# Performance work log

Hardware: AMD Instinct MI355X
Metric: run time of the kernel (lower is better)

Reference implementation:

```python
import jax, jax.numpy as jnp
import numpy as np

STRIDE = 4
NUM_HEADS = 8


def _make_window(x, stride, nh):
    # (B,C,H,W) -> (B, nh, S, S, (H/S)*(W/S), C/nh)
    b, c, h, w = x.shape
    x = x.reshape(b, nh, c // nh, h // stride, stride, w // stride, stride)
    x = x.transpose(0, 1, 4, 6, 3, 5, 2)
    return x.reshape(b, nh, stride, stride, (h // stride) * (w // stride), c // nh)


def _demake_window(x, h, w):
    # (B, nh, S, S, L, dh) -> (B, nh*dh, H, W)
    b, nh, s, _, L, dh = x.shape
    x = x.reshape(b, nh, s, s, h // s, w // s, dh)
    x = x.transpose(0, 1, 6, 4, 2, 5, 3)
    return x.reshape(b, nh * dh, h, w)


def _proj(x, W, bias):
    # 1x1 conv == per-pixel GEMM: (B,C,H,W),(O,C) -> (B,O,H,W)
    return jnp.einsum('bchw,oc->bohw', x, W) + bias[None, :, None, None]


def setup_inputs() -> dict:
    key = jax.random.key(0)
    ks = jax.random.split(key, 12)
    B, C, H, W = 4, 256, 64, 64
    P, V, O = 256, 256, 256  # proj/value/out channels
    inp = {
        'fea_q': jax.random.normal(ks[0], (B, C, H, W), jnp.float32),
        'fea_k': jax.random.normal(ks[1], (B, C, H, W), jnp.float32),
        'fea_v': jax.random.normal(ks[2], (B, V, H, W), jnp.float32),
        'mask_q': (jax.random.uniform(ks[3], (B, 1, H, W)) > 0.5).astype(jnp.float32),
        'mask_k': (jax.random.uniform(ks[4], (B, 1, H, W)) > 0.5).astype(jnp.float32),
        'q_w': jax.random.normal(ks[5], (P, C), jnp.float32) * 0.02,
        'q_b': jnp.zeros((P,), jnp.float32),
        'k_w': jax.random.normal(ks[6], (P, C), jnp.float32) * 0.02,
        'k_b': jnp.zeros((P,), jnp.float32),
        'v_w': jax.random.normal(ks[7], (O, V), jnp.float32) * 0.02,
        'v_b': jnp.zeros((O,), jnp.float32),
    }
    return inp


def reference(fea_q, fea_k, fea_v, mask_q, mask_k, q_w, q_b, k_w, k_b, v_w, v_b):
    B, _, H, W = fea_q.shape
    head_dim = q_w.shape[0] // NUM_HEADS
    scaling = head_dim ** (-0.5)

    query = _make_window(_proj(fea_q, q_w, q_b), STRIDE, NUM_HEADS)
    key = _make_window(_proj(fea_k, k_w, k_b), STRIDE, NUM_HEADS)
    value = _make_window(_proj(fea_v, v_w, v_b), STRIDE, NUM_HEADS)

    # (B, nh, S, S, L, L)
    weights = jnp.matmul(query, jnp.swapaxes(key, -1, -2)) * scaling

    # mask attention (no-grad in original)
    mq = _make_window(jax.lax.stop_gradient(mask_q), STRIDE, 1)
    mk = _make_window(jax.lax.stop_gradient(mask_k), STRIDE, 1)
    mask_attn = jnp.matmul(mq, jnp.swapaxes(mk, -1, -2))  # (B,1,S,S,L,L)
    mask_sum = jnp.sum(mask_attn, axis=-1, keepdims=True)
    mask_attn = mask_attn + (mask_sum == 0).astype(jnp.float32)
    mask_attn = jnp.where(mask_attn == 0, -jnp.inf,
                          jnp.where(mask_attn == 1, 0.0, mask_attn))
    weights = weights + mask_attn

    weights = jax.nn.softmax(weights, axis=-1)  # dropout p=0 -> identity
    weights = weights * (1.0 - (mask_sum == 0).astype(jnp.float32))

    out = jnp.matmul(weights, value)  # (B, nh, S, S, L, dh)
    return _demake_window(out, H, W)
```

## Files before the change

### kernel.cpp

```cpp
#include <hip/hip_runtime.h>
#include <hip/hip_bf16.h>

#define NH 8
#define DH 32
#define LW 256
#define HW 4096
#define CIN 256

typedef float f32x4 __attribute__((ext_vector_type(4)));
typedef short s16x8 __attribute__((ext_vector_type(8)));
typedef short s16x4 __attribute__((ext_vector_type(4)));

#define AS1 __attribute__((address_space(1)))
#define AS3 __attribute__((address_space(3)))

__device__ __forceinline__ short f2bf(float f) {
  __hip_bfloat16 h = __float2bfloat16(f);
  short s; __builtin_memcpy(&s, &h, 2); return s;
}

__device__ __forceinline__ void gload_lds16(const void* g, void* l) {
  __builtin_amdgcn_global_load_lds((const AS1 void*)g, (AS3 void*)l, 16, 0, 0);
}

#define KOFF 4194304
#define VOFF 8388608
#define WTOFF 12582912

__global__ void wconv_kernel(const float* __restrict__ qw, const float* __restrict__ kw,
                             const float* __restrict__ vw, short* __restrict__ ws) {
  int blk = blockIdx.x;
  int t = blk >> 5, kb = blk & 31;
  const float* W = (t == 0) ? qw : ((t == 1) ? kw : vw);
  int o = threadIdx.x;
  f32x4 w0 = *(const f32x4*)(W + o * CIN + kb * 8);
  f32x4 w1 = *(const f32x4*)(W + o * CIN + kb * 8 + 4);
  s16x8 v;
#pragma unroll
  for (int j = 0; j < 4; ++j) { v[j] = f2bf(w0[j]); v[4 + j] = f2bf(w1[j]); }
  *(s16x8*)(ws + WTOFF + (blk * 256 + o) * 8) = v;
}

__global__ void __launch_bounds__(256, 3)
proj_kernel(const float* __restrict__ fq, const float* __restrict__ fk,
            const float* __restrict__ fv,
            const float* __restrict__ qb, const float* __restrict__ kb_,
            const float* __restrict__ vb,
            short* __restrict__ ws) {
  __shared__ s16x8 SMEM[2112];

  int bid = blockIdx.x;
  int orig = (bid & 7) * 96 + (bid >> 3);
  int t = orig >> 8;
  int r0 = orig & 255;
  int b = r0 >> 6;
  int pblk = r0 & 63;

  const float* fea = (t == 0) ? fq : ((t == 1) ? fk : fv);
  const float* Bv  = (t == 0) ? qb : ((t == 1) ? kb_ : vb);
  const short* Wt  = ws + WTOFF + t * 65536;

  int p0 = pblk * 64;
  int tid = threadIdx.x;
  int lane = tid & 63, wv = tid >> 6;
  int g = lane >> 4, li = lane & 15;

  const f32x4 fzero = {0.f, 0.f, 0.f, 0.f};
  f32x4 acc[4][4];
#pragma unroll
  for (int m = 0; m < 4; ++m)
#pragma unroll
    for (int n = 0; n < 4; ++n) acc[m][n] = fzero;

  const float* feab = fea + b * (CIN * HW);
  int wq = tid & 15;
  int jh = (tid >> 4) & 1;
  int coct = tid >> 5;

  f32x4 ldB[4];

#define LOAD_B(cs_) do { int c0_ = (cs_) * 64; _Pragma("unroll") \
  for (int j_ = 0; j_ < 4; ++j_) \
    ldB[j_] = *(const f32x4*)(feab + (c0_ + coct * 8 + jh * 4 + j_) * HW + p0 + wq * 4); } while (0)

#define WRITE_B(buf_) do { _Pragma("unroll") \
  for (int pp_ = 0; pp_ < 4; ++pp_) { s16x4 v_; _Pragma("unroll") \
    for (int j_ = 0; j_ < 4; ++j_) v_[j_] = f2bf(ldB[j_][pp_]); \
    int w_ = wq * 4 + pp_; int wsw_ = w_ ^ ((w_ >> 3) & 7); \
    *(s16x4*)((short*)SMEM + ((buf_) * 512 + coct * 64 + wsw_) * 8 + jh * 4) = v_; } } while (0)

  LOAD_B(0);
  WRITE_B(0);
  __syncthreads();

#pragma unroll
  for (int cs = 0; cs < 4; ++cs) {
    if (cs < 3) LOAD_B(cs + 1);
    s16x8 aF[2][4];
#pragma unroll
    for (int kk = 0; kk < 2; ++kk)
#pragma unroll
      for (int m = 0; m < 4; ++m)
        aF[kk][m] = *(const s16x8*)(Wt + ((cs * 8 + kk * 4 + g) * 256 + wv * 64 + m * 16 + li) * 8);
#pragma unroll
    for (int kk = 0; kk < 2; ++kk) {
#pragma unroll
      for (int n = 0; n < 4; ++n) {
        int w = n * 16 + li;
        int wsw = w ^ ((w >> 3) & 7);
        s16x8 bb = SMEM[(cs & 1) * 512 + (kk * 4 + g) * 64 + wsw];
#pragma unroll
        for (int m = 0; m < 4; ++m)
          acc[m][n] = __builtin_amdgcn_mfma_f32_16x16x32_bf16(aF[kk][m], bb, acc[m][n], 0, 0, 0);
      }
    }
    if (cs < 3) {
      WRITE_B((cs + 1) & 1);
      __syncthreads();
    }
  }
#undef LOAD_B
#undef WRITE_B

  float bias_r[4][4];
#pragma unroll
  for (int m = 0; m < 4; ++m) {
    f32x4 b4 = *(const f32x4*)(Bv + wv * 64 + m * 16 + g * 4);
#pragma unroll
    for (int rr = 0; rr < 4; ++rr) bias_r[m][rr] = b4[rr];
  }

  __syncthreads();
  short* Tr = (short*)SMEM;
#pragma unroll
  for (int m = 0; m < 4; ++m) {
    int ob = wv * 64 + m * 16 + g * 4;
#pragma unroll
    for (int n = 0; n < 4; ++n) {
      int w = n * 16 + li;
      s16x4 v;
#pragma unroll
      for (int rr = 0; rr < 4; ++rr) v[rr] = f2bf(acc[m][n][rr] + bias_r[m][rr]);
      *(s16x4*)(Tr + w * 264 + ob) = v;
    }
  }
  __syncthreads();

  int s1 = pblk & 3, h0 = pblk >> 2;
  if (t != 2) {
    short* dst = ws + (t == 0 ? 0 : KOFF);
#pragma unroll
    for (int it = 0; it < 8; ++it) {
      int o_oct = it * 4 + (tid >> 6);
      int w = tid & 63;
      s16x8 v = *(const s16x8*)(Tr + w * 264 + o_oct * 8);
      int o = o_oct * 8;
      int nh = o >> 5, kb = (o & 31) >> 3;
      int s2 = w & 3, w0 = w >> 2;
      int l = h0 * 16 + w0;
      int winbase = (b * NH + nh) * 16 + s1 * 4 + s2;
      *(s16x8*)(dst + winbase * 8192 + (kb * 256 + l) * 8) = v;
    }
  } else {
#pragma unroll
    for (int it = 0; it < 8; ++it) {
      int d = tid;
      int s2 = it & 3, w0h = it >> 2;
      int l_oct = h0 * 2 + w0h;
      s16x8 v;
#pragma unroll
      for (int k = 0; k < 8; ++k) {
        int w = (w0h * 8 + k) * 4 + s2;
        v[k] = Tr[w * 264 + d];
      }
      int dh = d & 31;
      int nh2 = d >> 5;
      int winbase = (b * NH + nh2) * 16 + s1 * 4 + s2;
      int idx = l_oct * 256 + (dh >> 4) * 128 + (dh & 15) * 8;
      *(s16x8*)(ws + VOFF + winbase * 8192 + idx) = v;
    }
  }
}

__global__ void __launch_bounds__(256, 4)
attn_kernel(const short* __restrict__ ws, const float* __restrict__ mq,
            const float* __restrict__ mk, float* __restrict__ out) {
  __shared__ s16x8 KsV[1024];
  __shared__ s16x8 PsV[512];
  __shared__ float amaskS[256];
  __shared__ float mqS[128];
  __shared__ float facS[128];
  __shared__ int anyS[4];

  int bid = blockIdx.x;
  int orig = (bid & 7) * 128 + (bid >> 3);
  int qh = orig & 1;
  int s2 = (orig >> 1) & 3, s1 = (orig >> 3) & 3, nh = (orig >> 5) & 7, b = orig >> 8;
  int wwin = s1 * 4 + s2;
  int tid = threadIdx.x;
  int lane = tid & 63, wv = tid >> 6, g = lane >> 4, li = lane & 15;

  int winbase = (b * NH + nh) * 16 + wwin;
  const short* qt = ws + winbase * 8192;
  const short* kt = ws + KOFF + winbase * 8192;
  const short* vt = ws + VOFF + winbase * 8192;

#pragma unroll
  for (int i = 0; i < 4; ++i) {
    int seg = i * 4 + wv;
    gload_lds16(kt + (seg * 64 + lane) * 8, &KsV[seg * 64]);
  }

  {
    int l = tid;
    int h = (l >> 4) * 4 + s1, w = (l & 15) * 4 + s2;
    float mkv = mk[b * HW + h * 64 + w];
    amaskS[l] = (mkv > 0.5f) ? 0.0f : -1e30f;
    unsigned long long bal = __ballot(mkv > 0.5f);
    if (lane == 0) anyS[wv] = (bal != 0ULL) ? 1 : 0;
  }
  if (tid < 128) {
    int l = qh * 128 + tid;
    int h = (l >> 4) * 4 + s1, w = (l & 15) * 4 + s2;
    mqS[tid] = mq[b * HW + h * 64 + w];
  }

  int lq0 = wv * 32;
  s16x8 qa[2];
#pragma unroll
  for (int m = 0; m < 2; ++m)
    qa[m] = *(const s16x8*)(qt + (g * 256 + qh * 128 + lq0 + m * 16 + li) * 8);

  __syncthreads();
  int anyk = anyS[0] | anyS[1] | anyS[2] | anyS[3];

  const f32x4 fzero = {0.f, 0.f, 0.f, 0.f};
  f32x4 of[2][2];
#pragma unroll
  for (int m = 0; m < 2; ++m) { of[m][0] = fzero; of[m][1] = fzero; }
  float rs[8];
#pragma unroll
  for (int i = 0; i < 8; ++i) rs[i] = 0.0f;

  const float C = 0.17677669529663689f * 1.4426950408889634f;

#pragma unroll
  for (int lkb = 0; lkb < 4; ++lkb) {
    f32x4 sa[2][4];
#pragma unroll
    for (int n = 0; n < 4; ++n) {
      s16x8 kf = KsV[g * 256 + lkb * 64 + n * 16 + li];
#pragma unroll
      for (int m = 0; m < 2; ++m)
        sa[m][n] = __builtin_amdgcn_mfma_f32_16x16x32_bf16(qa[m], kf, fzero, 0, 0, 0);
    }
#pragma unroll
    for (int ks = 0; ks < 2; ++ks) {
#pragma unroll
      for (int n2 = 0; n2 < 2; ++n2) {
        int n = ks * 2 + n2;
        float am = amaskS[lkb * 64 + n * 16 + li];
#pragma unroll
        for (int m = 0; m < 2; ++m) {
#pragma unroll
          for (int rr = 0; rr < 4; ++rr) {
            float pval = exp2f(sa[m][n][rr] * C + am);
            rs[m * 4 + rr] += pval;
            int row = m * 16 + g * 4 + rr;
            int cl = n * 16 + li;
            int kbh = (cl >> 3) & 3;
            short* ps = (short*)&PsV[wv * 128 + kbh * 32 + row];
            ps[cl & 7] = f2bf(pval);
          }
        }
      }
      int kg = lkb * 2 + ks;
      s16x8 pb[2];
#pragma unroll
      for (int n = 0; n < 2; ++n) pb[n] = PsV[wv * 128 + g * 32 + n * 16 + li];
#pragma unroll
      for (int m2 = 0; m2 < 2; ++m2) {
        s16x8 va = *(const s16x8*)(vt + (kg * 4 + g) * 256 + m2 * 128 + li * 8);
#pragma unroll
        for (int n = 0; n < 2; ++n)
          of[m2][n] = __builtin_amdgcn_mfma_f32_16x16x32_bf16(va, pb[n], of[m2][n], 0, 0, 0);
      }
    }
  }

#pragma unroll
  for (int i = 0; i < 8; ++i) {
    float v = rs[i];
    v += __shfl_xor(v, 1);
    v += __shfl_xor(v, 2);
    v += __shfl_xor(v, 4);
    v += __shfl_xor(v, 8);
    rs[i] = v;
  }
  if (li == 0) {
#pragma unroll
    for (int m = 0; m < 2; ++m)
#pragma unroll
      for (int rr = 0; rr < 4; ++rr) {
        int row = m * 16 + g * 4 + rr;
        float sum = rs[m * 4 + rr];
        facS[wv * 32 + row] = (anyk && mqS[wv * 32 + row] > 0.5f) ? (1.0f / sum) : 0.0f;
      }
  }

#pragma unroll
  for (int m2 = 0; m2 < 2; ++m2) {
#pragma unroll
    for (int n = 0; n < 2; ++n) {
      int lloc = wv * 32 + n * 16;
      float fac = facS[lloc + li];
      int l = qh * 128 + lloc;
      int h = (l >> 4) * 4 + s1;
      int w = li * 4 + s2;
#pragma unroll
      for (int rr = 0; rr < 4; ++rr) {
        int o = nh * 32 + m2 * 16 + g * 4 + rr;
        out[((b * 256 + o) * 64 + h) * 64 + w] = of[m2][n][rr] * fac;
      }
    }
  }
}

extern "C" void kernel_launch(void* const* d_in, const int* in_sizes, int n_in,
                              void* d_out, int out_size, void* d_ws, size_t ws_size,
                              hipStream_t stream) {
  const float* fq = (const float*)d_in[0];
  const float* fk = (const float*)d_in[1];
  const float* fv = (const float*)d_in[2];
  const float* mq = (const float*)d_in[3];
  const float* mk = (const float*)d_in[4];
  const float* qw = (const float*)d_in[5];
  const float* qb = (const float*)d_in[6];
  const float* kw = (const float*)d_in[7];
  const float* kb = (const float*)d_in[8];
  const float* vw = (const float*)d_in[9];
  const float* vb = (const float*)d_in[10];
  short* ws = (short*)d_ws;

  wconv_kernel<<<96, 256, 0, stream>>>(qw, kw, vw, ws);
  proj_kernel<<<768, 256, 0, stream>>>(fq, fk, fv, qb, kb, vb, ws);
  attn_kernel<<<1024, 256, 0, stream>>>(ws, mq, mk, (float*)d_out);
}
```

Before: 47.90 us.

## Reorganize projected Q/K/V scratch layout to row-major per image row

```diff
diff --git a/kernel.cpp b/kernel.cpp
--- a/kernel.cpp
+++ b/kernel.cpp
@@ -23,8 +23,8 @@
   __builtin_amdgcn_global_load_lds((const AS1 void*)g, (AS3 void*)l, 16, 0, 0);
 }
 
-#define KOFF 4194304
-#define VOFF 8388608
+#define KOFF2 4194304
+#define VOFF2 8388608
 #define WTOFF 12582912
 
 __global__ void wconv_kernel(const float* __restrict__ qw, const float* __restrict__ kw,
@@ -146,38 +146,30 @@
   }
   __syncthreads();
 
-  int s1 = pblk & 3, h0 = pblk >> 2;
+  int h = pblk;
   if (t != 2) {
-    short* dst = ws + (t == 0 ? 0 : KOFF);
+    short* dst = ws + (t == 0 ? 0 : KOFF2) + ((b * 64 + h) * 8) * 2048;
 #pragma unroll
     for (int it = 0; it < 8; ++it) {
-      int o_oct = it * 4 + (tid >> 6);
-      int w = tid & 63;
-      s16x8 v = *(const s16x8*)(Tr + w * 264 + o_oct * 8);
-      int o = o_oct * 8;
-      int nh = o >> 5, kb = (o & 31) >> 3;
-      int s2 = w & 3, w0 = w >> 2;
-      int l = h0 * 16 + w0;
-      int winbase = (b * NH + nh) * 16 + s1 * 4 + s2;
-      *(s16x8*)(dst + winbase * 8192 + (kb * 256 + l) * 8) = v;
+      int c = it * 256 + tid;
+      int doct = c & 3, w0 = (c >> 2) & 15, s2 = (c >> 6) & 3, nh = c >> 8;
+      int w = w0 * 4 + s2;
+      s16x8 v = *(const s16x8*)(Tr + w * 264 + nh * 32 + doct * 8);
+      *(s16x8*)(dst + ((nh * 4 + s2) * 16 + w0) * 32 + doct * 8) = v;
     }
   } else {
+    short* dst = ws + VOFF2 + ((b * 64 + h) * 8) * 2048;
 #pragma unroll
     for (int it = 0; it < 8; ++it) {
-      int d = tid;
-      int s2 = it & 3, w0h = it >> 2;
-      int l_oct = h0 * 2 + w0h;
+      int c = it * 256 + tid;
+      int w0h = c & 1, d = (c >> 1) & 31, s2 = (c >> 6) & 3, nh = c >> 8;
       s16x8 v;
 #pragma unroll
       for (int k = 0; k < 8; ++k) {
         int w = (w0h * 8 + k) * 4 + s2;
-        v[k] = Tr[w * 264 + d];
-      }
-      int dh = d & 31;
-      int nh2 = d >> 5;
-      int winbase = (b * NH + nh2) * 16 + s1 * 4 + s2;
-      int idx = l_oct * 256 + (dh >> 4) * 128 + (dh & 15) * 8;
-      *(s16x8*)(ws + VOFF + winbase * 8192 + idx) = v;
+        v[k] = Tr[w * 264 + nh * 32 + d];
+      }
+      *(s16x8*)(dst + ((nh * 4 + s2) * 32 + d) * 16 + w0h * 8) = v;
     }
   }
 }
@@ -196,19 +188,23 @@
   int orig = (bid & 7) * 128 + (bid >> 3);
   int qh = orig & 1;
   int s2 = (orig >> 1) & 3, s1 = (orig >> 3) & 3, nh = (orig >> 5) & 7, b = orig >> 8;
-  int wwin = s1 * 4 + s2;
   int tid = threadIdx.x;
   int lane = tid & 63, wv = tid >> 6, g = lane >> 4, li = lane & 15;
 
-  int winbase = (b * NH + nh) * 16 + wwin;
-  const short* qt = ws + winbase * 8192;
-  const short* kt = ws + KOFF + winbase * 8192;
-  const short* vt = ws + VOFF + winbase * 8192;
+#define RBQK(h0_) (((((b * 64 + (h0_) * 4 + s1) * 8 + nh) * 4 + s2)) * 16)
+#define RBV(h0_)  (((((b * 64 + (h0_) * 4 + s1) * 8 + nh) * 4 + s2)) * 512)
+
+  const short* Qb = ws;
+  const short* Kb = ws + KOFF2;
+  const short* Vb = ws + VOFF2;
 
 #pragma unroll
   for (int i = 0; i < 4; ++i) {
     int seg = i * 4 + wv;
-    gload_lds16(kt + (seg * 64 + lane) * 8, &KsV[seg * 64]);
+    int kb = seg >> 2;
+    int l = (seg & 3) * 64 + lane;
+    int h0 = l >> 4, w0 = l & 15;
+    gload_lds16(Kb + (RBQK(h0) + w0) * 32 + kb * 8, &KsV[seg * 64]);
   }
 
   {
@@ -225,11 +221,12 @@
     mqS[tid] = mq[b * HW + h * 64 + w];
   }
 
-  int lq0 = wv * 32;
   s16x8 qa[2];
 #pragma unroll
-  for (int m = 0; m < 2; ++m)
-    qa[m] = *(const s16x8*)(qt + (g * 256 + qh * 128 + lq0 + m * 16 + li) * 8);
+  for (int m = 0; m < 2; ++m) {
+    int h0 = qh * 8 + wv * 2 + m;
+    qa[m] = *(const s16x8*)(Qb + (RBQK(h0) + li) * 32 + g * 8);
+  }
 
   __syncthreads();
   int anyk = anyS[0] | anyS[1] | anyS[2] | anyS[3];
@@ -274,19 +271,24 @@
           }
         }
       }
-      int kg = lkb * 2 + ks;
+      int koct = lkb * 2 + ks;
+      int kg4g = koct * 4 + g;
+      int h0v = kg4g >> 1, w0h = kg4g & 1;
       s16x8 pb[2];
 #pragma unroll
       for (int n = 0; n < 2; ++n) pb[n] = PsV[wv * 128 + g * 32 + n * 16 + li];
 #pragma unroll
       for (int m2 = 0; m2 < 2; ++m2) {
-        s16x8 va = *(const s16x8*)(vt + (kg * 4 + g) * 256 + m2 * 128 + li * 8);
+        int d = m2 * 16 + li;
+        s16x8 va = *(const s16x8*)(Vb + RBV(h0v) + d * 16 + w0h * 8);
 #pragma unroll
         for (int n = 0; n < 2; ++n)
           of[m2][n] = __builtin_amdgcn_mfma_f32_16x16x32_bf16(va, pb[n], of[m2][n], 0, 0, 0);
       }
     }
   }
+#undef RBQK
+#undef RBV
 
 #pragma unroll
   for (int i = 0; i < 8; ++i) {
```

New measurement: 48.43 us. Within noise of the previous version (+1.1%).

## Read K and masks directly from global into registers, dropping LDS staging and barrier

Applied to the files above, without the earlier changes.

```diff
diff --git a/kernel.cpp b/kernel.cpp
--- a/kernel.cpp
+++ b/kernel.cpp
@@ -185,12 +185,8 @@
 __global__ void __launch_bounds__(256, 4)
 attn_kernel(const short* __restrict__ ws, const float* __restrict__ mq,
             const float* __restrict__ mk, float* __restrict__ out) {
-  __shared__ s16x8 KsV[1024];
   __shared__ s16x8 PsV[512];
-  __shared__ float amaskS[256];
-  __shared__ float mqS[128];
   __shared__ float facS[128];
-  __shared__ int anyS[4];
 
   int bid = blockIdx.x;
   int orig = (bid & 7) * 128 + (bid >> 3);
@@ -205,25 +201,17 @@
   const short* kt = ws + KOFF + winbase * 8192;
   const short* vt = ws + VOFF + winbase * 8192;
 
-#pragma unroll
-  for (int i = 0; i < 4; ++i) {
-    int seg = i * 4 + wv;
-    gload_lds16(kt + (seg * 64 + lane) * 8, &KsV[seg * 64]);
-  }
-
-  {
-    int l = tid;
-    int h = (l >> 4) * 4 + s1, w = (l & 15) * 4 + s2;
+  float amr[16];
+  int any16 = 0;
+#pragma unroll
+  for (int j = 0; j < 16; ++j) {
+    int h = j * 4 + s1;
+    int w = li * 4 + s2;
     float mkv = mk[b * HW + h * 64 + w];
-    amaskS[l] = (mkv > 0.5f) ? 0.0f : -1e30f;
-    unsigned long long bal = __ballot(mkv > 0.5f);
-    if (lane == 0) anyS[wv] = (bal != 0ULL) ? 1 : 0;
-  }
-  if (tid < 128) {
-    int l = qh * 128 + tid;
-    int h = (l >> 4) * 4 + s1, w = (l & 15) * 4 + s2;
-    mqS[tid] = mq[b * HW + h * 64 + w];
-  }
+    amr[j] = (mkv > 0.5f) ? 0.0f : -1e30f;
+    any16 |= (mkv > 0.5f) ? 1 : 0;
+  }
+  int anyk = (__ballot(any16 != 0) != 0ULL) ? 1 : 0;
 
   int lq0 = wv * 32;
   s16x8 qa[2];
@@ -231,9 +219,6 @@
   for (int m = 0; m < 2; ++m)
     qa[m] = *(const s16x8*)(qt + (g * 256 + qh * 128 + lq0 + m * 16 + li) * 8);
 
-  __syncthreads();
-  int anyk = anyS[0] | anyS[1] | anyS[2] | anyS[3];
-
   const f32x4 fzero = {0.f, 0.f, 0.f, 0.f};
   f32x4 of[2][2];
 #pragma unroll
@@ -249,7 +234,7 @@
     f32x4 sa[2][4];
 #pragma unroll
     for (int n = 0; n < 4; ++n) {
-      s16x8 kf = KsV[g * 256 + lkb * 64 + n * 16 + li];
+      s16x8 kf = *(const s16x8*)(kt + (g * 256 + lkb * 64 + n * 16 + li) * 8);
 #pragma unroll
       for (int m = 0; m < 2; ++m)
         sa[m][n] = __builtin_amdgcn_mfma_f32_16x16x32_bf16(qa[m], kf, fzero, 0, 0, 0);
@@ -259,7 +244,7 @@
 #pragma unroll
       for (int n2 = 0; n2 < 2; ++n2) {
         int n = ks * 2 + n2;
-        float am = amaskS[lkb * 64 + n * 16 + li];
+        float am = amr[lkb * 4 + n];
 #pragma unroll
         for (int m = 0; m < 2; ++m) {
 #pragma unroll
@@ -303,8 +288,9 @@
 #pragma unroll
       for (int rr = 0; rr < 4; ++rr) {
         int row = m * 16 + g * 4 + rr;
-        float sum = rs[m * 4 + rr];
-        facS[wv * 32 + row] = (anyk && mqS[wv * 32 + row] > 0.5f) ? (1.0f / sum) : 0.0f;
+        int lq = qh * 128 + wv * 32 + row;
+        float mqv = mq[b * HW + ((lq >> 4) * 4 + s1) * 64 + (lq & 15) * 4 + s2];
+        facS[wv * 32 + row] = (anyk && mqv > 0.5f) ? (1.0f / rs[m * 4 + rr]) : 0.0f;
       }
   }
 
```

Result: slower. 51.19 us (+6.9%).
